# Kernel optimization log

Measured on AMD Instinct MI355X. Metric: run time of the kernel, lower is better.

Reference implementation:

```python
import jax, jax.numpy as jnp
import numpy as np

EPS = 1e-5


def setup_inputs() -> dict:
    key = jax.random.key(0)
    k1, k2, k3 = jax.random.split(key, 3)
    B, C, H, W = 64, 512, 28, 28
    G = 8
    x = jax.random.normal(k1, (B, C, H, W), dtype=jnp.float32)
    weight = jax.random.normal(k2, (G,), dtype=jnp.float32)
    bias = jax.random.normal(k3, (G,), dtype=jnp.float32)
    return {"x": x, "weight": weight, "bias": bias, "groups": G}


def reference(x, weight, bias, groups):
    B, C, H, W = x.shape
    G = groups
    cpg = C // G
    hw = H * W
    xg = x.reshape(B, G, cpg, hw)                       # [B,G,cpg,HW]
    # per-channel spatial mean
    means = jnp.mean(xg, axis=-1, keepdims=True)        # [B,G,cpg,1]
    # similarity map: dot product of each spatial vector with channel-mean vector
    s = jnp.sum(xg * means, axis=2)                     # [B,G,HW]
    # normalize s over spatial dim (population variance, eps=1e-5)
    mu = jnp.mean(s, axis=-1, keepdims=True)
    var = jnp.mean(jnp.square(s - mu), axis=-1, keepdims=True)
    t = (s - mu) * jax.lax.rsqrt(var + EPS)             # [B,G,HW]
    gate = jax.nn.sigmoid(t * weight[None, :, None] + bias[None, :, None])
    out = xg * gate[:, :, None, :]                      # broadcast gate over channels
    return out.reshape(B, C, H, W)
```

## Files before the change

### kernel.cpp

```cpp
#include <hip/hip_runtime.h>


#define HW      784
#define NG      8
#define TILE_F  50176
#define TILE4   12544
#define CHUNK_F 6272
#define NCH     8

typedef float    f32x4 __attribute__((ext_vector_type(4)));
typedef _Float16 f16x4 __attribute__((ext_vector_type(4)));

#define XH_OFF    0
#define ST_OFF    100352
#define GB_OFF    150528
#define SM_OFF    153664
#define RED_OFF   153696
#define LDS_TOTAL 153760

__device__ __forceinline__ void gload16(const float* g, float* l) {
    __builtin_amdgcn_global_load_lds(
        (const __attribute__((address_space(1))) void*)g,
        (__attribute__((address_space(3))) void*)l, 16, 0, 0);
}

#define WAIT_VM(N)  asm volatile("s_waitcnt vmcnt(" #N ")" ::: "memory")
#define WAIT_LGKM() asm volatile("s_waitcnt lgkmcnt(0)" ::: "memory")
#define RAW_BAR()   do { __builtin_amdgcn_s_barrier(); \
                         __builtin_amdgcn_sched_barrier(0); } while (0)

__global__ __launch_bounds__(512, 1)
void sge_kernel(const float* __restrict__ x, const float* __restrict__ weight,
                const float* __restrict__ bias, float* __restrict__ out) {
    extern __shared__ char smem[];
    _Float16* xh   = (_Float16*)(smem + XH_OFF);
    float*    stg  = (float*)(smem + ST_OFF);
    float*    gbuf = (float*)(smem + GB_OFF);
    float*    smean= (float*)(smem + SM_OFF);
    float*    red  = (float*)(smem + RED_OFF);

    const int t = threadIdx.x, lane = t & 63, wave = t >> 6;
    const int bg = blockIdx.x, g = bg & (NG - 1);
    const float* xt = x + (size_t)bg * TILE_F;
    const bool has1 = t < (HW - 512);

    auto issue = [&](int e, int b) {
        const float* gs = xt + e * CHUNK_F;
        float* ld = stg + b * CHUNK_F;
        const int uo = wave * 768;
        gload16(gs + uo       + lane * 4, ld + uo);
        gload16(gs + uo + 256 + lane * 4, ld + uo + 256);
        gload16(gs + uo + 512 + lane * 4, ld + uo + 512);
        if (wave == 0 && lane < 32)
            gload16(gs + 6144 + lane * 4, ld + 6144);
    };

    issue(0, 0);
    issue(1, 1);

    float acc0 = 0.f, acc1 = 0.f;

    for (int e = 0; e < NCH; ++e) {
        const int b = e & 1;
        if (e < NCH - 1) { if (wave == 0) WAIT_VM(4); else WAIT_VM(3); }
        else             { WAIT_VM(0); }
        RAW_BAR();

        {
            const f32x4* r4 = (const f32x4*)(stg + b * CHUNK_F + wave * HW);
            const f32x4 v0 = r4[lane], v1 = r4[lane + 64], v2 = r4[lane + 128];
            float s = ((v0.x + v0.y) + (v0.z + v0.w))
                    + ((v1.x + v1.y) + (v1.z + v1.w))
                    + ((v2.x + v2.y) + (v2.z + v2.w));
            if (lane < 4) {
                const f32x4 v3 = r4[lane + 192];
                s += (v3.x + v3.y) + (v3.z + v3.w);
            }
#pragma unroll
            for (int m = 1; m < 64; m <<= 1) s += __shfl_xor(s, m, 64);
            if (lane == 0) smean[wave] = s * (1.0f / (float)HW);
        }
        WAIT_LGKM(); RAW_BAR();

        {
            const float* sb = stg + b * CHUNK_F;
            const float m0 = smean[0], m1 = smean[1], m2 = smean[2], m3 = smean[3];
            const float m4 = smean[4], m5 = smean[5], m6 = smean[6], m7 = smean[7];
            acc0 += sb[t]          * m0 + sb[t + HW]     * m1
                  + sb[t + 2 * HW] * m2 + sb[t + 3 * HW] * m3
                  + sb[t + 4 * HW] * m4 + sb[t + 5 * HW] * m5
                  + sb[t + 6 * HW] * m6 + sb[t + 7 * HW] * m7;
            if (has1) {
                const int p = t + 512;
                acc1 += sb[p]          * m0 + sb[p + HW]     * m1
                      + sb[p + 2 * HW] * m2 + sb[p + 3 * HW] * m3
                      + sb[p + 4 * HW] * m4 + sb[p + 5 * HW] * m5
                      + sb[p + 6 * HW] * m6 + sb[p + 7 * HW] * m7;
            }
            const f32x4* s4 = (const f32x4*)sb;
            f16x4* x4h = (f16x4*)xh + e * 1568;
            x4h[t]        = __builtin_convertvector(s4[t],        f16x4);
            x4h[t + 512]  = __builtin_convertvector(s4[t + 512],  f16x4);
            x4h[t + 1024] = __builtin_convertvector(s4[t + 1024], f16x4);
            if (t < 32)
                x4h[t + 1536] = __builtin_convertvector(s4[t + 1536], f16x4);
        }
        WAIT_LGKM(); RAW_BAR();
        if (e + 2 < NCH) issue(e + 2, b);
    }

    float rs  = acc0 + (has1 ? acc1 : 0.f);
    float rs2 = acc0 * acc0 + (has1 ? acc1 * acc1 : 0.f);
#pragma unroll
    for (int m = 1; m < 64; m <<= 1) {
        rs  += __shfl_xor(rs,  m, 64);
        rs2 += __shfl_xor(rs2, m, 64);
    }
    if (lane == 0) { red[wave] = rs; red[8 + wave] = rs2; }
    __syncthreads();
    float ss = 0.f, ss2 = 0.f;
#pragma unroll
    for (int w = 0; w < 8; ++w) { ss += red[w]; ss2 += red[8 + w]; }
    const float mu   = ss * (1.0f / (float)HW);
    const float var  = ss2 * (1.0f / (float)HW) - mu * mu;
    const float rstd = rsqrtf(var + 1e-5f);
    const float wg   = weight[g];
    const float bv   = bias[g];

    gbuf[t] = 1.0f / (1.0f + __expf(-((acc0 - mu) * rstd * wg + bv)));
    if (has1)
        gbuf[t + 512] = 1.0f / (1.0f + __expf(-((acc1 - mu) * rstd * wg + bv)));
    __syncthreads();

    const f16x4* x4h = (const f16x4*)xh;
    const f32x4* gb4 = (const f32x4*)gbuf;
    f32x4* o4 = (f32x4*)(out + (size_t)bg * TILE_F);
    int col = t % 196;
#pragma unroll
    for (int r = 0; r < 24; ++r) {
        const int idx = t + r * 512;
        const f32x4 xv = __builtin_convertvector(x4h[idx], f32x4);
        o4[idx] = xv * gb4[col];
        col += 120; if (col >= 196) col -= 196;
    }
    if (t < 256) {
        const int idx = 12288 + t;
        const f32x4 xv = __builtin_convertvector(x4h[idx], f32x4);
        o4[idx] = xv * gb4[idx % 196];
    }
}

extern "C" void kernel_launch(void* const* d_in, const int* in_sizes, int n_in,
                              void* d_out, int out_size, void* d_ws, size_t ws_size,
                              hipStream_t stream) {
    const float* x      = (const float*)d_in[0];
    const float* weight = (const float*)d_in[1];
    const float* bias   = (const float*)d_in[2];
    float* out = (float*)d_out;

    static bool init = false;
    if (!init) {
        (void)hipFuncSetAttribute((const void*)sge_kernel,
                                  hipFuncAttributeMaxDynamicSharedMemorySize,
                                  LDS_TOTAL);
        init = true;
    }
    sge_kernel<<<dim3(512), dim3(512), LDS_TOTAL, stream>>>(x, weight, bias, out);
}
```

Before: 190.6 us.

## Keep fp16 tile copy in registers instead of LDS to cut shared memory

The fp16 copy of each 8-channel chunk now lives in per-thread registers (pk0/pk1/pk2 arrays plus one tail value) instead of a 100KB LDS buffer. The chunk loop is fully unrolled, and each thread's gate values are loaded once before the output loop. LDS use drops to about 50KB and becomes static, so the launch bound allows several blocks per CU and the one-time dynamic shared memory setup is removed. The cost is higher register pressure, with 25 f16x4 values held per thread.

```diff
diff --git a/kernel.cpp b/kernel.cpp
--- a/kernel.cpp
+++ b/kernel.cpp
@@ -4,19 +4,12 @@
 #define HW      784
 #define NG      8
 #define TILE_F  50176
-#define TILE4   12544
 #define CHUNK_F 6272
+#define CH4     1568
 #define NCH     8
 
 typedef float    f32x4 __attribute__((ext_vector_type(4)));
 typedef _Float16 f16x4 __attribute__((ext_vector_type(4)));
-
-#define XH_OFF    0
-#define ST_OFF    100352
-#define GB_OFF    150528
-#define SM_OFF    153664
-#define RED_OFF   153696
-#define LDS_TOTAL 153760
 
 __device__ __forceinline__ void gload16(const float* g, float* l) {
     __builtin_amdgcn_global_load_lds(
@@ -29,24 +22,23 @@
 #define RAW_BAR()   do { __builtin_amdgcn_s_barrier(); \
                          __builtin_amdgcn_sched_barrier(0); } while (0)
 
-__global__ __launch_bounds__(512, 1)
+__global__ __launch_bounds__(512, 4)
 void sge_kernel(const float* __restrict__ x, const float* __restrict__ weight,
                 const float* __restrict__ bias, float* __restrict__ out) {
-    extern __shared__ char smem[];
-    _Float16* xh   = (_Float16*)(smem + XH_OFF);
-    float*    stg  = (float*)(smem + ST_OFF);
-    float*    gbuf = (float*)(smem + GB_OFF);
-    float*    smean= (float*)(smem + SM_OFF);
-    float*    red  = (float*)(smem + RED_OFF);
+    __shared__ float stg[2][CHUNK_F];
+    __shared__ float gbuf[HW];
+    __shared__ float smean[8];
+    __shared__ float red[16];
 
     const int t = threadIdx.x, lane = t & 63, wave = t >> 6;
     const int bg = blockIdx.x, g = bg & (NG - 1);
     const float* xt = x + (size_t)bg * TILE_F;
     const bool has1 = t < (HW - 512);
+    const int  tc   = t >> 5;
 
     auto issue = [&](int e, int b) {
         const float* gs = xt + e * CHUNK_F;
-        float* ld = stg + b * CHUNK_F;
+        float* ld = stg[b];
         const int uo = wave * 768;
         gload16(gs + uo       + lane * 4, ld + uo);
         gload16(gs + uo + 256 + lane * 4, ld + uo + 256);
@@ -59,7 +51,9 @@
     issue(1, 1);
 
     float acc0 = 0.f, acc1 = 0.f;
+    f16x4 pk0[NCH], pk1[NCH], pk2[NCH], pt;
 
+#pragma unroll
     for (int e = 0; e < NCH; ++e) {
         const int b = e & 1;
         if (e < NCH - 1) { if (wave == 0) WAIT_VM(4); else WAIT_VM(3); }
@@ -67,7 +61,7 @@
         RAW_BAR();
 
         {
-            const f32x4* r4 = (const f32x4*)(stg + b * CHUNK_F + wave * HW);
+            const f32x4* r4 = (const f32x4*)(stg[b] + wave * HW);
             const f32x4 v0 = r4[lane], v1 = r4[lane + 64], v2 = r4[lane + 128];
             float s = ((v0.x + v0.y) + (v0.z + v0.w))
                     + ((v1.x + v1.y) + (v1.z + v1.w))
@@ -83,7 +77,7 @@
         WAIT_LGKM(); RAW_BAR();
 
         {
-            const float* sb = stg + b * CHUNK_F;
+            const float* sb = stg[b];
             const float m0 = smean[0], m1 = smean[1], m2 = smean[2], m3 = smean[3];
             const float m4 = smean[4], m5 = smean[5], m6 = smean[6], m7 = smean[7];
             acc0 += sb[t]          * m0 + sb[t + HW]     * m1
@@ -98,12 +92,11 @@
                       + sb[p + 6 * HW] * m6 + sb[p + 7 * HW] * m7;
             }
             const f32x4* s4 = (const f32x4*)sb;
-            f16x4* x4h = (f16x4*)xh + e * 1568;
-            x4h[t]        = __builtin_convertvector(s4[t],        f16x4);
-            x4h[t + 512]  = __builtin_convertvector(s4[t + 512],  f16x4);
-            x4h[t + 1024] = __builtin_convertvector(s4[t + 1024], f16x4);
-            if (t < 32)
-                x4h[t + 1536] = __builtin_convertvector(s4[t + 1536], f16x4);
+            pk0[e] = __builtin_convertvector(s4[t],        f16x4);
+            pk1[e] = __builtin_convertvector(s4[t + 512],  f16x4);
+            pk2[e] = __builtin_convertvector(s4[t + 1024], f16x4);
+            if (t < 256 && tc == e)
+                pt = __builtin_convertvector(s4[1536 + (t & 31)], f16x4);
         }
         WAIT_LGKM(); RAW_BAR();
         if (e + 2 < NCH) issue(e + 2, b);
@@ -132,21 +125,20 @@
         gbuf[t + 512] = 1.0f / (1.0f + __expf(-((acc1 - mu) * rstd * wg + bv)));
     __syncthreads();
 
-    const f16x4* x4h = (const f16x4*)xh;
     const f32x4* gb4 = (const f32x4*)gbuf;
+    const f32x4 g0 = gb4[t % 196];
+    const f32x4 g1 = gb4[(t + 512) % 196];
+    const f32x4 g2 = gb4[(t + 1024) % 196];
     f32x4* o4 = (f32x4*)(out + (size_t)bg * TILE_F);
-    int col = t % 196;
 #pragma unroll
-    for (int r = 0; r < 24; ++r) {
-        const int idx = t + r * 512;
-        const f32x4 xv = __builtin_convertvector(x4h[idx], f32x4);
-        o4[idx] = xv * gb4[col];
-        col += 120; if (col >= 196) col -= 196;
+    for (int e = 0; e < NCH; ++e) {
+        o4[e * CH4 + t]        = __builtin_convertvector(pk0[e], f32x4) * g0;
+        o4[e * CH4 + t + 512]  = __builtin_convertvector(pk1[e], f32x4) * g1;
+        o4[e * CH4 + t + 1024] = __builtin_convertvector(pk2[e], f32x4) * g2;
     }
     if (t < 256) {
-        const int idx = 12288 + t;
-        const f32x4 xv = __builtin_convertvector(x4h[idx], f32x4);
-        o4[idx] = xv * gb4[idx % 196];
+        const int q = 1536 + (t & 31);
+        o4[tc * CH4 + q] = __builtin_convertvector(pt, f32x4) * gb4[q % 196];
     }
 }
 
@@ -157,13 +149,5 @@
     const float* weight = (const float*)d_in[1];
     const float* bias   = (const float*)d_in[2];
     float* out = (float*)d_out;
-
-    static bool init = false;
-    if (!init) {
-        (void)hipFuncSetAttribute((const void*)sge_kernel,
-                                  hipFuncAttributeMaxDynamicSharedMemorySize,
-                                  LDS_TOTAL);
-        init = true;
-    }
-    sge_kernel<<<dim3(512), dim3(512), LDS_TOTAL, stream>>>(x, weight, bias, out);
+    sge_kernel<<<dim3(512), dim3(512), 0, stream>>>(x, weight, bias, out);
 }
```

Result: slower. 251.1 us (+31.7%).

## Process two groups per 1024-thread block, overlapping first group's stores with second's loads

Applied to the files above, without the earlier changes.

Each block now handles two (batch, group) tiles sequentially with 1024 threads and 256 blocks. The output writes for the first tile are interleaved into the chunk loop of the second tile's loads, so stores overlap with incoming global-to-LDS traffic instead of running as a separate tail phase. Only the second tile's writeback remains at the end. The risks are the per-block serial dependency across two tiles, the fp16 staging reused between tiles, and halving the grid, which leaves fewer blocks to spread across CUs.

```diff
diff --git a/kernel.cpp b/kernel.cpp
--- a/kernel.cpp
+++ b/kernel.cpp
@@ -4,9 +4,10 @@
 #define HW      784
 #define NG      8
 #define TILE_F  50176
-#define TILE4   12544
 #define CHUNK_F 6272
+#define CH4     1568
 #define NCH     8
+#define NGC     16
 
 typedef float    f32x4 __attribute__((ext_vector_type(4)));
 typedef _Float16 f16x4 __attribute__((ext_vector_type(4)));
@@ -16,7 +17,7 @@
 #define GB_OFF    150528
 #define SM_OFF    153664
 #define RED_OFF   153696
-#define LDS_TOTAL 153760
+#define LDS_TOTAL 153824
 
 __device__ __forceinline__ void gload16(const float* g, float* l) {
     __builtin_amdgcn_global_load_lds(
@@ -24,49 +25,82 @@
         (__attribute__((address_space(3))) void*)l, 16, 0, 0);
 }
 
-#define WAIT_VM(N)  asm volatile("s_waitcnt vmcnt(" #N ")" ::: "memory")
 #define WAIT_LGKM() asm volatile("s_waitcnt lgkmcnt(0)" ::: "memory")
 #define RAW_BAR()   do { __builtin_amdgcn_s_barrier(); \
                          __builtin_amdgcn_sched_barrier(0); } while (0)
 
-__global__ __launch_bounds__(512, 1)
+__device__ __forceinline__ void wait_vm_n(int n) {
+    if (n == 0)      asm volatile("s_waitcnt vmcnt(0)" ::: "memory");
+    else if (n == 1) asm volatile("s_waitcnt vmcnt(1)" ::: "memory");
+    else if (n == 2) asm volatile("s_waitcnt vmcnt(2)" ::: "memory");
+    else             asm volatile("s_waitcnt vmcnt(4)" ::: "memory");
+}
+
+__global__ __launch_bounds__(1024, 4)
 void sge_kernel(const float* __restrict__ x, const float* __restrict__ weight,
                 const float* __restrict__ bias, float* __restrict__ out) {
     extern __shared__ char smem[];
-    _Float16* xh   = (_Float16*)(smem + XH_OFF);
-    float*    stg  = (float*)(smem + ST_OFF);
-    float*    gbuf = (float*)(smem + GB_OFF);
-    float*    smean= (float*)(smem + SM_OFF);
-    float*    red  = (float*)(smem + RED_OFF);
+    _Float16* xh    = (_Float16*)(smem + XH_OFF);
+    float*    stg   = (float*)(smem + ST_OFF);
+    float*    gbuf  = (float*)(smem + GB_OFF);
+    float*    smean = (float*)(smem + SM_OFF);
+    float*    red   = (float*)(smem + RED_OFF);
 
     const int t = threadIdx.x, lane = t & 63, wave = t >> 6;
-    const int bg = blockIdx.x, g = bg & (NG - 1);
-    const float* xt = x + (size_t)bg * TILE_F;
-    const bool has1 = t < (HW - 512);
+    const int blk  = blockIdx.x;
+    const int col0 = t % 196;
+    const int col1 = (t + 44) % 196;
 
-    auto issue = [&](int e, int b) {
-        const float* gs = xt + e * CHUNK_F;
-        float* ld = stg + b * CHUNK_F;
-        const int uo = wave * 768;
-        gload16(gs + uo       + lane * 4, ld + uo);
-        gload16(gs + uo + 256 + lane * 4, ld + uo + 256);
-        gload16(gs + uo + 512 + lane * 4, ld + uo + 512);
-        if (wave == 0 && lane < 32)
-            gload16(gs + 6144 + lane * 4, ld + 6144);
+    float wg = weight[blk & 7];
+    float bv = bias[blk & 7];
+    asm volatile("" : "+v"(wg), "+v"(bv));
+
+    auto issue = [&](int gc) {
+        const int bg = blk + ((gc >> 3) << 8);
+        const float* gs = x + (size_t)bg * TILE_F + (size_t)(gc & 7) * CHUNK_F;
+        float* ld = stg + (gc & 1) * CHUNK_F;
+        if (wave < 8) {
+            gload16(gs + wave * 256 + lane * 4, ld + wave * 256);
+            gload16(gs + 4096 + wave * 256 + lane * 4, ld + 4096 + wave * 256);
+        } else if (wave == 8) {
+            gload16(gs + 2048 + lane * 4, ld + 2048);
+            if (lane < 32) gload16(gs + 6144 + lane * 4, ld + 6144);
+        } else {
+            gload16(gs + wave * 256 + lane * 4, ld + wave * 256);
+        }
     };
 
-    issue(0, 0);
-    issue(1, 1);
+    issue(0); issue(1);
 
-    float acc0 = 0.f, acc1 = 0.f;
+    float acc = 0.f;
+    f32x4 ga0 = {0.f, 0.f, 0.f, 0.f}, ga1 = {0.f, 0.f, 0.f, 0.f};
 
-    for (int e = 0; e < NCH; ++e) {
-        const int b = e & 1;
-        if (e < NCH - 1) { if (wave == 0) WAIT_VM(4); else WAIT_VM(3); }
-        else             { WAIT_VM(0); }
+#pragma unroll
+    for (int gc = 0; gc < NGC; ++gc) {
+        const int  b  = gc & 1, e = gc & 7;
+        const bool t1 = gc >= 8;
+
+        if (t1) {
+            const f16x4* px = (const f16x4*)xh + e * CH4;
+            f32x4* o4 = (f32x4*)(out + (size_t)blk * TILE_F) + e * CH4;
+            o4[t] = __builtin_convertvector(px[t], f32x4) * ga0;
+            if (wave < 8) {
+                o4[1024 + t] = __builtin_convertvector(px[1024 + t], f32x4) * ga1;
+            } else if (wave == 8) {
+                if (lane < 32)
+                    o4[1024 + t] = __builtin_convertvector(px[1024 + t], f32x4) * ga1;
+            }
+        }
+
+        {
+            const bool hn = (gc <= 14);
+            const int  n  = (wave <= 8) ? ((hn ? 2 : 0) + (t1 ? 2 : 0))
+                                        : ((hn ? 1 : 0) + (t1 ? 1 : 0));
+            wait_vm_n(n);
+        }
         RAW_BAR();
 
-        {
+        if (wave < 8) {
             const f32x4* r4 = (const f32x4*)(stg + b * CHUNK_F + wave * HW);
             const f32x4 v0 = r4[lane], v1 = r4[lane + 64], v2 = r4[lane + 128];
             float s = ((v0.x + v0.y) + (v0.z + v0.w))
@@ -84,69 +118,65 @@
 
         {
             const float* sb = stg + b * CHUNK_F;
-            const float m0 = smean[0], m1 = smean[1], m2 = smean[2], m3 = smean[3];
-            const float m4 = smean[4], m5 = smean[5], m6 = smean[6], m7 = smean[7];
-            acc0 += sb[t]          * m0 + sb[t + HW]     * m1
-                  + sb[t + 2 * HW] * m2 + sb[t + 3 * HW] * m3
-                  + sb[t + 4 * HW] * m4 + sb[t + 5 * HW] * m5
-                  + sb[t + 6 * HW] * m6 + sb[t + 7 * HW] * m7;
-            if (has1) {
-                const int p = t + 512;
-                acc1 += sb[p]          * m0 + sb[p + HW]     * m1
-                      + sb[p + 2 * HW] * m2 + sb[p + 3 * HW] * m3
-                      + sb[p + 4 * HW] * m4 + sb[p + 5 * HW] * m5
-                      + sb[p + 6 * HW] * m6 + sb[p + 7 * HW] * m7;
+            if (t < HW) {
+                float a = 0.f;
+#pragma unroll
+                for (int r = 0; r < 8; ++r) a += sb[t + r * HW] * smean[r];
+                acc += a;
             }
             const f32x4* s4 = (const f32x4*)sb;
-            f16x4* x4h = (f16x4*)xh + e * 1568;
-            x4h[t]        = __builtin_convertvector(s4[t],        f16x4);
-            x4h[t + 512]  = __builtin_convertvector(s4[t + 512],  f16x4);
-            x4h[t + 1024] = __builtin_convertvector(s4[t + 1024], f16x4);
-            if (t < 32)
-                x4h[t + 1536] = __builtin_convertvector(s4[t + 1536], f16x4);
+            f16x4* px = (f16x4*)xh + e * CH4;
+            px[t] = __builtin_convertvector(s4[t], f16x4);
+            if (wave < 8) {
+                px[1024 + t] = __builtin_convertvector(s4[1024 + t], f16x4);
+            } else if (wave == 8) {
+                if (lane < 32)
+                    px[1024 + t] = __builtin_convertvector(s4[1024 + t], f16x4);
+            }
         }
         WAIT_LGKM(); RAW_BAR();
-        if (e + 2 < NCH) issue(e + 2, b);
+        if (gc + 2 < NGC) issue(gc + 2);
+
+        if (e == 7) {
+            float rs  = (t < HW) ? acc : 0.f;
+            float rs2 = rs * rs;
+#pragma unroll
+            for (int m = 1; m < 64; m <<= 1) {
+                rs  += __shfl_xor(rs,  m, 64);
+                rs2 += __shfl_xor(rs2, m, 64);
+            }
+            if (lane == 0) { red[wave] = rs; red[16 + wave] = rs2; }
+            WAIT_LGKM(); RAW_BAR();
+            float ss = 0.f, ss2 = 0.f;
+#pragma unroll
+            for (int w = 0; w < 16; ++w) { ss += red[w]; ss2 += red[16 + w]; }
+            const float mu   = ss * (1.0f / (float)HW);
+            const float var  = ss2 * (1.0f / (float)HW) - mu * mu;
+            const float rstd = rsqrtf(var + 1e-5f);
+            if (t < HW)
+                gbuf[t] = 1.0f / (1.0f + __expf(-((acc - mu) * rstd * wg + bv)));
+            WAIT_LGKM(); RAW_BAR();
+            const f32x4* gb4 = (const f32x4*)gbuf;
+            ga0 = gb4[col0];
+            ga1 = gb4[col1];
+            acc = 0.f;
+        }
     }
 
-    float rs  = acc0 + (has1 ? acc1 : 0.f);
-    float rs2 = acc0 * acc0 + (has1 ? acc1 * acc1 : 0.f);
+    {
+        f32x4* o4t = (f32x4*)(out + (size_t)(blk + 256) * TILE_F);
 #pragma unroll
-    for (int m = 1; m < 64; m <<= 1) {
-        rs  += __shfl_xor(rs,  m, 64);
-        rs2 += __shfl_xor(rs2, m, 64);
-    }
-    if (lane == 0) { red[wave] = rs; red[8 + wave] = rs2; }
-    __syncthreads();
-    float ss = 0.f, ss2 = 0.f;
-#pragma unroll
-    for (int w = 0; w < 8; ++w) { ss += red[w]; ss2 += red[8 + w]; }
-    const float mu   = ss * (1.0f / (float)HW);
-    const float var  = ss2 * (1.0f / (float)HW) - mu * mu;
-    const float rstd = rsqrtf(var + 1e-5f);
-    const float wg   = weight[g];
-    const float bv   = bias[g];
-
-    gbuf[t] = 1.0f / (1.0f + __expf(-((acc0 - mu) * rstd * wg + bv)));
-    if (has1)
-        gbuf[t + 512] = 1.0f / (1.0f + __expf(-((acc1 - mu) * rstd * wg + bv)));
-    __syncthreads();
-
-    const f16x4* x4h = (const f16x4*)xh;
-    const f32x4* gb4 = (const f32x4*)gbuf;
-    f32x4* o4 = (f32x4*)(out + (size_t)bg * TILE_F);
-    int col = t % 196;
-#pragma unroll
-    for (int r = 0; r < 24; ++r) {
-        const int idx = t + r * 512;
-        const f32x4 xv = __builtin_convertvector(x4h[idx], f32x4);
-        o4[idx] = xv * gb4[col];
-        col += 120; if (col >= 196) col -= 196;
-    }
-    if (t < 256) {
-        const int idx = 12288 + t;
-        const f32x4 xv = __builtin_convertvector(x4h[idx], f32x4);
-        o4[idx] = xv * gb4[idx % 196];
+        for (int e = 0; e < NCH; ++e) {
+            const f16x4* px = (const f16x4*)xh + e * CH4;
+            f32x4* o4 = o4t + e * CH4;
+            o4[t] = __builtin_convertvector(px[t], f32x4) * ga0;
+            if (wave < 8) {
+                o4[1024 + t] = __builtin_convertvector(px[1024 + t], f32x4) * ga1;
+            } else if (wave == 8) {
+                if (lane < 32)
+                    o4[1024 + t] = __builtin_convertvector(px[1024 + t], f32x4) * ga1;
+            }
+        }
     }
 }
 
@@ -165,5 +195,5 @@
                                   LDS_TOTAL);
         init = true;
     }
-    sge_kernel<<<dim3(512), dim3(512), LDS_TOTAL, stream>>>(x, weight, bias, out);
+    sge_kernel<<<dim3(256), dim3(1024), LDS_TOTAL, stream>>>(x, weight, bias, out);
 }
```

Measured after the change: 187.6 us. No clear change (-1.6%).

## Give each wave private channel rows to drop per-chunk block barriers

Applied to the files above, without the earlier changes.

Each wave now streams its own 8 channel rows through a private double-buffered LDS slot. It computes the channel mean with a wave shuffle and accumulates the similarity map in registers, so the three block-wide barriers per chunk go away. The per-wave partial similarity maps are reduced once through LDS at the end. This trades barrier stalls for extra register pressure from four vector accumulators and one extra LDS reduction pass.

```diff
diff --git a/kernel.cpp b/kernel.cpp
--- a/kernel.cpp
+++ b/kernel.cpp
@@ -2,10 +2,9 @@
 
 
 #define HW      784
+#define HW4     196
 #define NG      8
 #define TILE_F  50176
-#define TILE4   12544
-#define CHUNK_F 6272
 #define NCH     8
 
 typedef float    f32x4 __attribute__((ext_vector_type(4)));
@@ -14,9 +13,8 @@
 #define XH_OFF    0
 #define ST_OFF    100352
 #define GB_OFF    150528
-#define SM_OFF    153664
-#define RED_OFF   153696
-#define LDS_TOTAL 153760
+#define RED_OFF   153664
+#define LDS_TOTAL 153728
 
 __device__ __forceinline__ void gload16(const float* g, float* l) {
     __builtin_amdgcn_global_load_lds(
@@ -24,7 +22,6 @@
         (__attribute__((address_space(3))) void*)l, 16, 0, 0);
 }
 
-#define WAIT_VM(N)  asm volatile("s_waitcnt vmcnt(" #N ")" ::: "memory")
 #define WAIT_LGKM() asm volatile("s_waitcnt lgkmcnt(0)" ::: "memory")
 #define RAW_BAR()   do { __builtin_amdgcn_s_barrier(); \
                          __builtin_amdgcn_sched_barrier(0); } while (0)
@@ -36,117 +33,116 @@
     _Float16* xh   = (_Float16*)(smem + XH_OFF);
     float*    stg  = (float*)(smem + ST_OFF);
     float*    gbuf = (float*)(smem + GB_OFF);
-    float*    smean= (float*)(smem + SM_OFF);
     float*    red  = (float*)(smem + RED_OFF);
 
     const int t = threadIdx.x, lane = t & 63, wave = t >> 6;
     const int bg = blockIdx.x, g = bg & (NG - 1);
     const float* xt = x + (size_t)bg * TILE_F;
-    const bool has1 = t < (HW - 512);
 
-    auto issue = [&](int e, int b) {
-        const float* gs = xt + e * CHUNK_F;
-        float* ld = stg + b * CHUNK_F;
-        const int uo = wave * 768;
-        gload16(gs + uo       + lane * 4, ld + uo);
-        gload16(gs + uo + 256 + lane * 4, ld + uo + 256);
-        gload16(gs + uo + 512 + lane * 4, ld + uo + 512);
-        if (wave == 0 && lane < 32)
-            gload16(gs + 6144 + lane * 4, ld + 6144);
+    float wg = weight[g], bv = bias[g];
+    asm volatile("" : "+v"(wg), "+v"(bv));
+
+    const int wrow = wave * NCH;
+    float* slot0 = stg + (wave * 2) * HW;
+    float* slot1 = stg + (wave * 2 + 1) * HW;
+
+    auto issue_row = [&](int r) {
+        const float* gs = xt + (size_t)(wrow + r) * HW;
+        float* ld = (r & 1) ? slot1 : slot0;
+        gload16(gs + lane * 4,       ld);
+        gload16(gs + 256 + lane * 4, ld + 256);
+        gload16(gs + 512 + lane * 4, ld + 512);
+        if (lane < 4) gload16(gs + 768 + lane * 4, ld + 768);
     };
 
-    issue(0, 0);
-    issue(1, 1);
+    issue_row(0);
+    issue_row(1);
 
-    float acc0 = 0.f, acc1 = 0.f;
+    f32x4 acc0 = {0.f,0.f,0.f,0.f}, acc1 = {0.f,0.f,0.f,0.f};
+    f32x4 acc2 = {0.f,0.f,0.f,0.f}, acc3 = {0.f,0.f,0.f,0.f};
 
-    for (int e = 0; e < NCH; ++e) {
-        const int b = e & 1;
-        if (e < NCH - 1) { if (wave == 0) WAIT_VM(4); else WAIT_VM(3); }
-        else             { WAIT_VM(0); }
-        RAW_BAR();
+#pragma unroll
+    for (int r = 0; r < NCH; ++r) {
+        if (r < NCH - 1) asm volatile("s_waitcnt vmcnt(4)" ::: "memory");
+        else             asm volatile("s_waitcnt vmcnt(0)" ::: "memory");
+        __builtin_amdgcn_sched_barrier(0);
 
-        {
-            const f32x4* r4 = (const f32x4*)(stg + b * CHUNK_F + wave * HW);
-            const f32x4 v0 = r4[lane], v1 = r4[lane + 64], v2 = r4[lane + 128];
-            float s = ((v0.x + v0.y) + (v0.z + v0.w))
-                    + ((v1.x + v1.y) + (v1.z + v1.w))
-                    + ((v2.x + v2.y) + (v2.z + v2.w));
-            if (lane < 4) {
-                const f32x4 v3 = r4[lane + 192];
-                s += (v3.x + v3.y) + (v3.z + v3.w);
-            }
+        const f32x4* s4 = (const f32x4*)((r & 1) ? slot1 : slot0);
+        const f32x4 v0 = s4[lane], v1 = s4[lane + 64], v2 = s4[lane + 128];
+        f32x4 v3 = {0.f,0.f,0.f,0.f};
+        if (lane < 4) v3 = s4[192 + lane];
+
+        float m = ((v0.x + v0.y) + (v0.z + v0.w))
+                + ((v1.x + v1.y) + (v1.z + v1.w))
+                + ((v2.x + v2.y) + (v2.z + v2.w))
+                + ((v3.x + v3.y) + (v3.z + v3.w));
 #pragma unroll
-            for (int m = 1; m < 64; m <<= 1) s += __shfl_xor(s, m, 64);
-            if (lane == 0) smean[wave] = s * (1.0f / (float)HW);
-        }
-        WAIT_LGKM(); RAW_BAR();
+        for (int d = 1; d < 64; d <<= 1) m += __shfl_xor(m, d, 64);
+        m *= (1.0f / (float)HW);
 
-        {
-            const float* sb = stg + b * CHUNK_F;
-            const float m0 = smean[0], m1 = smean[1], m2 = smean[2], m3 = smean[3];
-            const float m4 = smean[4], m5 = smean[5], m6 = smean[6], m7 = smean[7];
-            acc0 += sb[t]          * m0 + sb[t + HW]     * m1
-                  + sb[t + 2 * HW] * m2 + sb[t + 3 * HW] * m3
-                  + sb[t + 4 * HW] * m4 + sb[t + 5 * HW] * m5
-                  + sb[t + 6 * HW] * m6 + sb[t + 7 * HW] * m7;
-            if (has1) {
-                const int p = t + 512;
-                acc1 += sb[p]          * m0 + sb[p + HW]     * m1
-                      + sb[p + 2 * HW] * m2 + sb[p + 3 * HW] * m3
-                      + sb[p + 4 * HW] * m4 + sb[p + 5 * HW] * m5
-                      + sb[p + 6 * HW] * m6 + sb[p + 7 * HW] * m7;
-            }
-            const f32x4* s4 = (const f32x4*)sb;
-            f16x4* x4h = (f16x4*)xh + e * 1568;
-            x4h[t]        = __builtin_convertvector(s4[t],        f16x4);
-            x4h[t + 512]  = __builtin_convertvector(s4[t + 512],  f16x4);
-            x4h[t + 1024] = __builtin_convertvector(s4[t + 1024], f16x4);
-            if (t < 32)
-                x4h[t + 1536] = __builtin_convertvector(s4[t + 1536], f16x4);
-        }
-        WAIT_LGKM(); RAW_BAR();
-        if (e + 2 < NCH) issue(e + 2, b);
+        acc0 += m * v0; acc1 += m * v1; acc2 += m * v2; acc3 += m * v3;
+
+        f16x4* ph = (f16x4*)xh + (wrow + r) * HW4;
+        ph[lane]       = __builtin_convertvector(v0, f16x4);
+        ph[lane + 64]  = __builtin_convertvector(v1, f16x4);
+        ph[lane + 128] = __builtin_convertvector(v2, f16x4);
+        if (lane < 4) ph[192 + lane] = __builtin_convertvector(v3, f16x4);
+
+        __builtin_amdgcn_sched_barrier(0);
+        if (r + 2 < NCH) issue_row(r + 2);
     }
 
-    float rs  = acc0 + (has1 ? acc1 : 0.f);
-    float rs2 = acc0 * acc0 + (has1 ? acc1 * acc1 : 0.f);
+    WAIT_LGKM(); RAW_BAR();
+    {
+        f32x4* cw = (f32x4*)(stg + wave * HW);
+        cw[lane] = acc0; cw[lane + 64] = acc1; cw[lane + 128] = acc2;
+        if (lane < 4) cw[192 + lane] = acc3;
+    }
+    WAIT_LGKM(); RAW_BAR();
+
+    const bool has1 = t < (HW - 512);
+    float s0 = 0.f, s1 = 0.f;
 #pragma unroll
-    for (int m = 1; m < 64; m <<= 1) {
-        rs  += __shfl_xor(rs,  m, 64);
-        rs2 += __shfl_xor(rs2, m, 64);
+    for (int w = 0; w < 8; ++w) {
+        s0 += stg[w * HW + t];
+        if (has1) s1 += stg[w * HW + t + 512];
+    }
+
+    float rs  = s0 + (has1 ? s1 : 0.f);
+    float rs2 = s0 * s0 + (has1 ? s1 * s1 : 0.f);
+#pragma unroll
+    for (int d = 1; d < 64; d <<= 1) {
+        rs  += __shfl_xor(rs,  d, 64);
+        rs2 += __shfl_xor(rs2, d, 64);
     }
     if (lane == 0) { red[wave] = rs; red[8 + wave] = rs2; }
-    __syncthreads();
+    WAIT_LGKM(); RAW_BAR();
+
     float ss = 0.f, ss2 = 0.f;
 #pragma unroll
     for (int w = 0; w < 8; ++w) { ss += red[w]; ss2 += red[8 + w]; }
     const float mu   = ss * (1.0f / (float)HW);
     const float var  = ss2 * (1.0f / (float)HW) - mu * mu;
     const float rstd = rsqrtf(var + 1e-5f);
-    const float wg   = weight[g];
-    const float bv   = bias[g];
 
-    gbuf[t] = 1.0f / (1.0f + __expf(-((acc0 - mu) * rstd * wg + bv)));
+    gbuf[t] = 1.0f / (1.0f + __expf(-((s0 - mu) * rstd * wg + bv)));
     if (has1)
-        gbuf[t + 512] = 1.0f / (1.0f + __expf(-((acc1 - mu) * rstd * wg + bv)));
-    __syncthreads();
+        gbuf[t + 512] = 1.0f / (1.0f + __expf(-((s1 - mu) * rstd * wg + bv)));
+    WAIT_LGKM(); RAW_BAR();
 
-    const f16x4* x4h = (const f16x4*)xh;
     const f32x4* gb4 = (const f32x4*)gbuf;
+    const f16x4* px  = (const f16x4*)xh;
     f32x4* o4 = (f32x4*)(out + (size_t)bg * TILE_F);
-    int col = t % 196;
+    int col = t % HW4;
 #pragma unroll
-    for (int r = 0; r < 24; ++r) {
-        const int idx = t + r * 512;
-        const f32x4 xv = __builtin_convertvector(x4h[idx], f32x4);
-        o4[idx] = xv * gb4[col];
-        col += 120; if (col >= 196) col -= 196;
+    for (int rr = 0; rr < 24; ++rr) {
+        const int idx = t + rr * 512;
+        o4[idx] = __builtin_convertvector(px[idx], f32x4) * gb4[col];
+        col += 120; if (col >= HW4) col -= HW4;
     }
     if (t < 256) {
         const int idx = 12288 + t;
-        const f32x4 xv = __builtin_convertvector(x4h[idx], f32x4);
-        o4[idx] = xv * gb4[idx % 196];
+        o4[idx] = __builtin_convertvector(px[idx], f32x4) * gb4[idx % HW4];
     }
 }
 
```

Measured after the change: 189.9 us. No clear change (-0.4%).
